# Kernel optimization log

Measured on AMD Instinct MI355X. Metric: run time of the kernel, lower is better.

## Reference

```python
import jax, jax.numpy as jnp
import numpy as np

D_MODEL = 1024
NUM_HEADS = 16
HEAD_DIM = D_MODEL // NUM_HEADS
WINDOW = 64
GLOBAL_TOKENS = 4
MAX_SEQ_LEN = 2048
RANDOM_TOKENS = 32
BATCH = 2
SEQ = 2048
NEG = -1.0e9
LN_EPS = 1e-5


def setup_inputs() -> dict:
    key = jax.random.key(0)
    k1, k2, k3, k4 = jax.random.split(key, 4)
    x = jax.random.normal(k1, (BATCH, SEQ, D_MODEL), dtype=jnp.float32)
    w_qkv = jax.random.normal(k2, (D_MODEL, 3 * D_MODEL), dtype=jnp.float32) * (D_MODEL ** -0.5)
    w_out = jax.random.normal(k3, (D_MODEL, D_MODEL), dtype=jnp.float32) * (D_MODEL ** -0.5)
    ln_gamma = jnp.ones((D_MODEL,), dtype=jnp.float32)
    ln_beta = jnp.zeros((D_MODEL,), dtype=jnp.float32)
    rand_idx = jax.random.randint(k4, (MAX_SEQ_LEN, RANDOM_TOKENS), 0, MAX_SEQ_LEN, dtype=jnp.int32)
    return {"x": x, "w_qkv": w_qkv, "w_out": w_out,
            "ln_gamma": ln_gamma, "ln_beta": ln_beta, "rand_idx": rand_idx}


def _build_masks(seq_len, rand_idx):
    i = jnp.arange(seq_len)
    causal = (i[:, None] >= i[None, :]).astype(jnp.float32)  # [L,L], lower-triangular
    # local window mask
    dist = jnp.abs(i[:, None] - i[None, :])
    local = (dist <= WINDOW).astype(jnp.float32) * causal
    # global column mask: columns {0..G-1} u {L-G..L-1}, rows i >= g (== causal on those cols)
    gcols = jnp.concatenate([jnp.arange(GLOBAL_TOKENS), jnp.arange(seq_len - GLOBAL_TOKENS, seq_len)])
    is_gcol = jnp.zeros((seq_len,), jnp.float32).at[gcols].set(1.0)
    glob = is_gcol[None, :] * causal
    # random mask: per-row fixed random columns, then causal-filtered
    ri = rand_idx[:seq_len]  # [L, R]
    rows = jnp.broadcast_to(i[:, None], ri.shape)
    rnd = jnp.zeros((seq_len, seq_len), jnp.float32).at[rows, ri].set(1.0) * causal
    return local, glob, rnd


def reference(x, w_qkv, w_out, ln_gamma, ln_beta, rand_idx):
    B, L, _ = x.shape
    residual = x
    # LayerNorm
    mu = jnp.mean(x, axis=-1, keepdims=True)
    var = jnp.mean(jnp.square(x - mu), axis=-1, keepdims=True)
    xn = (x - mu) * jax.lax.rsqrt(var + LN_EPS) * ln_gamma + ln_beta
    # QKV projection
    qkv = xn @ w_qkv
    q, k, v = jnp.split(qkv, 3, axis=-1)
    q = q.reshape(B, L, NUM_HEADS, HEAD_DIM).transpose(0, 2, 1, 3)  # [B,H,L,D]
    k = k.reshape(B, L, NUM_HEADS, HEAD_DIM).transpose(0, 2, 1, 3)
    v = v.reshape(B, L, NUM_HEADS, HEAD_DIM).transpose(0, 2, 1, 3)
    local, glob, rnd = _build_masks(L, rand_idx)
    raw = jnp.einsum('bhqd,bhkd->bhqk', q, k) / jnp.sqrt(jnp.float32(HEAD_DIM))
    # original sums three masked copies of the same scores:
    # combined = 3*raw + ((1-local)+(1-glob)+(1-rnd)) * NEG
    penalty = (3.0 - (local + glob + rnd)) * NEG  # [L,L]
    combined = 3.0 * raw + penalty[None, None, :, :]
    attn = jax.nn.softmax(combined, axis=-1)
    out = jnp.einsum('bhqk,bhkd->bhqd', attn, v)
    out = out.transpose(0, 2, 1, 3).reshape(B, L, D_MODEL)
    out = out @ w_out
    return out + residual
```

## Files before the change

### kernel.cpp

```cpp
#include <hip/hip_runtime.h>
#include <stdint.h>

typedef __attribute__((ext_vector_type(8))) short shortx8;
typedef __attribute__((ext_vector_type(4))) float floatx4;

static constexpr int SEQ_    = 2048;
static constexpr int DMODEL  = 1024;
static constexpr int HDIM    = 64;
static constexpr int BATCH_  = 2;
static constexpr int NHEADS  = 16;
static constexpr int WINDOW_ = 64;
static constexpr int GTOK    = 4;
static constexpr int RTOK    = 32;
static constexpr int ROWS    = BATCH_ * SEQ_;
static constexpr int QKVN    = 3 * DMODEL;

__device__ inline unsigned short f2bf(float f) {
  union { float f; unsigned int u; } x; x.f = f;
  unsigned int r = (x.u + 0x7FFFu + ((x.u >> 16) & 1u)) >> 16;
  return (unsigned short)r;
}
__device__ inline float bf2f(unsigned short b) {
  union { unsigned int u; float f; } x; x.u = ((unsigned int)b) << 16;
  return x.f;
}

__device__ inline void gload_lds16(const void* g, void* l) {
  __builtin_amdgcn_global_load_lds(
      (const __attribute__((address_space(1))) void*)g,
      (__attribute__((address_space(3))) void*)l, 16, 0, 0);
}

__device__ __forceinline__ void gemm_core128(
    const unsigned short* __restrict__ aSrc0, const unsigned short* __restrict__ aSrc1,
    const unsigned short* __restrict__ bSrc0, const unsigned short* __restrict__ bSrc1,
    unsigned short* Al, unsigned short* Bl,
    const int wave, const int lane, floatx4 (&acc)[4][4]) {
  const int quad = lane >> 4, l16 = lane & 15;
  const int wm = (wave >> 1) * 64, wn = (wave & 1) * 64;
  unsigned short* AlD0 = Al + (wave * 32) * 32;
  unsigned short* AlD1 = AlD0 + 16 * 32;
  unsigned short* BlD0 = Bl + (wave * 32) * 32;
  unsigned short* BlD1 = BlD0 + 16 * 32;
  for (int k0 = 0; k0 < 1024; k0 += 32) {
    __syncthreads();
    gload_lds16(aSrc0 + k0, AlD0);
    gload_lds16(aSrc1 + k0, AlD1);
    gload_lds16(bSrc0 + k0, BlD0);
    gload_lds16(bSrc1 + k0, BlD1);
    __syncthreads();
    shortx8 af[4], bfr[4];
    #pragma unroll
    for (int s = 0; s < 4; s++)
      af[s] = *(const shortx8*)&Al[(wm + s * 16 + l16) * 32 + quad * 8];
    #pragma unroll
    for (int s = 0; s < 4; s++)
      bfr[s] = *(const shortx8*)&Bl[(wn + s * 16 + l16) * 32 + quad * 8];
    #pragma unroll
    for (int sm = 0; sm < 4; sm++)
      #pragma unroll
      for (int sn = 0; sn < 4; sn++)
        acc[sm][sn] = __builtin_amdgcn_mfma_f32_16x16x32_bf16(af[sm], bfr[sn], acc[sm][sn], 0, 0, 0);
  }
}

__global__ __launch_bounds__(256) void k1_prep(
    const float* __restrict__ x, const float* __restrict__ w_qkv,
    const float* __restrict__ w_out, const float* __restrict__ gamma,
    const float* __restrict__ beta, const int* __restrict__ ridx,
    unsigned short* __restrict__ xn, unsigned short* __restrict__ wqT,
    unsigned short* __restrict__ woT, unsigned short* __restrict__ Wvs,
    int* __restrict__ cols, int* __restrict__ cnt, int* __restrict__ tmx,
    int* __restrict__ cnts2, int* __restrict__ qlist) {
  __shared__ float tile[32][33];
  __shared__ float red[4], red2[4];
  __shared__ int rl[RTOK];
  __shared__ int scw, scnw, stm;
  const int bx = blockIdx.x;
  const int t = threadIdx.x;
  if (bx < 3072) {
    int n0 = (bx % 96) * 32, k0 = (bx / 96) * 32;
    int tx = t & 31, ty = t >> 5;
    #pragma unroll
    for (int r = ty; r < 32; r += 8)
      tile[r][tx] = w_qkv[(size_t)(k0 + r) * QKVN + n0 + tx];
    __syncthreads();
    #pragma unroll
    for (int r = ty; r < 32; r += 8)
      wqT[(size_t)(n0 + r) * DMODEL + k0 + tx] = f2bf(tile[tx][r]);
  } else if (bx < 7168) {
    int row = bx - 3072;
    const float4* xr = (const float4*)(x + (size_t)row * DMODEL);
    float4 v = xr[t];
    float s = v.x + v.y + v.z + v.w;
    #pragma unroll
    for (int o = 32; o > 0; o >>= 1) s += __shfl_xor(s, o);
    int wave = t >> 6, lane = t & 63;
    if (lane == 0) red[wave] = s;
    __syncthreads();
    float mean = (red[0] + red[1] + red[2] + red[3]) * (1.0f / DMODEL);
    float dx = v.x - mean, dy = v.y - mean, dz = v.z - mean, dw = v.w - mean;
    float q = dx*dx + dy*dy + dz*dz + dw*dw;
    #pragma unroll
    for (int o = 32; o > 0; o >>= 1) q += __shfl_xor(q, o);
    if (lane == 0) red2[wave] = q;
    __syncthreads();
    float var = (red2[0] + red2[1] + red2[2] + red2[3]) * (1.0f / DMODEL);
    float rs = rsqrtf(var + 1e-5f);
    float4 g = ((const float4*)gamma)[t];
    float4 bb = ((const float4*)beta)[t];
    ushort4 outv;
    outv.x = f2bf(dx * rs * g.x + bb.x);
    outv.y = f2bf(dy * rs * g.y + bb.y);
    outv.z = f2bf(dz * rs * g.z + bb.z);
    outv.w = f2bf(dw * rs * g.w + bb.w);
    ((ushort4*)(xn + (size_t)row * DMODEL))[t] = outv;
  } else if (bx < 8192) {
    int idx = bx - 7168;
    int n0 = (idx & 31) * 32, k0 = (idx >> 5) * 32;
    int tx = t & 31, ty = t >> 5;
    #pragma unroll
    for (int r = ty; r < 32; r += 8)
      tile[r][tx] = w_out[(size_t)(k0 + r) * DMODEL + n0 + tx];
    __syncthreads();
    #pragma unroll
    for (int r = ty; r < 32; r += 8)
      woT[(size_t)(n0 + r) * DMODEL + k0 + tx] = f2bf(tile[tx][r]);
  } else if (bx < 9216) {
    int idx = bx - 8192;
    int v0 = (idx & 31) * 32, k0 = (idx >> 5) * 32;
    int tx = t & 31, ty = t >> 5;
    #pragma unroll
    for (int r = ty; r < 32; r += 8)
      Wvs[(size_t)(k0 + r) * DMODEL + v0 + tx] =
          f2bf(w_qkv[(size_t)(k0 + r) * QKVN + 2 * DMODEL + v0 + tx]);
  } else {
    const int i = bx - 9216;
    if (t < RTOK) rl[t] = ridx[i * RTOK + t];
    if (t == 0) { scw = 0; scnw = 0; stm = 0; }
    __syncthreads();
    const int wstart = (i - WINDOW_ > 0) ? (i - WINDOW_) : 0;
    const int c = t;
    int j = -1;
    bool valid = false;
    bool iswin = (c < 65);
    if (c < 65) {
      j = i - WINDOW_ + c;
      valid = (j >= 0);
    } else if (c < 73) {
      int g = c - 65;
      j = (g < 4) ? g : (SEQ_ - 8 + g);
      valid = (j <= i) && (j < wstart);
    } else if (c < 73 + RTOK) {
      int r = c - 73;
      j = rl[r];
      bool dup = false;
      for (int r2 = 0; r2 < r; r2++) dup = dup || (rl[r2] == j);
      valid = (j <= i) && (j < wstart) && !(j < GTOK || j >= SEQ_ - GTOK) && !dup;
    }
    int tier = -1;
    if (valid) {
      int loc = ((i - j) <= WINDOW_) ? 1 : 0;
      int glb = (j < GTOK || j >= SEQ_ - GTOK) ? 1 : 0;
      int rnd = 0;
      for (int r = 0; r < RTOK; r++) rnd |= (rl[r] == j) ? 1 : 0;
      tier = loc + glb + rnd;
      atomicMax(&stm, tier);
    }
    __syncthreads();
    const int tm = stm;
    if (valid && tier == tm) {
      if (iswin) {
        int pos = atomicAdd(&scw, 1);
        cols[i * 128 + pos] = j;
      } else {
        int pos = 127 - atomicAdd(&scnw, 1);
        cols[i * 128 + pos] = j;
      }
    }
    __syncthreads();
    if (t == 0) {
      cnt[i] = scw + scnw;
      tmx[i] = tm;
      cnts2[i] = scw | (scnw << 16);
      if (i < 68 || i >= SEQ_ - 4) {
        int cc = (i < 68) ? i : 68 + (i - (SEQ_ - 4));
        qlist[cc * 2 + 0] = (tm == 3) ? i : -1;
        qlist[cc * 2 + 1] = (tm == 3) ? (SEQ_ + i) : -1;
      }
    }
  }
}

__global__ __launch_bounds__(256) void k2_fused(
    const unsigned short* __restrict__ xn, const int* __restrict__ cols,
    const int* __restrict__ tmx, const int* __restrict__ cnts2,
    const unsigned short* __restrict__ woT, const unsigned short* __restrict__ Wvs,
    const unsigned short* __restrict__ wqT, const int* __restrict__ qlist,
    unsigned short* __restrict__ WvoT, unsigned short* __restrict__ qf,
    unsigned short* __restrict__ kf, unsigned short* __restrict__ vf,
    unsigned short* __restrict__ xbar) {
  __shared__ __align__(16) unsigned short smem[80 * 256];
  const int bx = blockIdx.x, t = threadIdx.x;
  const int wave = t >> 6, lane = t & 63;
  if (bx < 96) {
    unsigned short* Al = smem;
    unsigned short* Bl = smem + 128 * 32;
    const int lrow = lane >> 2, lkoff = (lane & 3) * 8;
    const int quad = lane >> 4, l16 = lane & 15;
    const int wm = (wave >> 1) * 64, wn = (wave & 1) * 64;
    floatx4 acc[4][4] = {};
    if (bx < 64) {
      const int bm = (bx >> 3) * 128, bn = (bx & 7) * 128;
      const unsigned short* a0 = woT + (size_t)(bm + wave * 32 + lrow) * DMODEL + lkoff;
      const unsigned short* a1 = a0 + 16 * DMODEL;
      const unsigned short* b0 = Wvs + (size_t)(bn + wave * 32 + lrow) * DMODEL + lkoff;
      const unsigned short* b1 = b0 + 16 * DMODEL;
      gemm_core128(a0, a1, b0, b1, Al, Bl, wave, lane, acc);
      #pragma unroll
      for (int sm = 0; sm < 4; sm++)
        #pragma unroll
        for (int sn = 0; sn < 4; sn++)
          #pragma unroll
          for (int r = 0; r < 4; r++) {
            int row = bm + wm + sm * 16 + quad * 4 + r;
            int col = bn + wn + sn * 16 + l16;
            WvoT[(size_t)row * DMODEL + col] = f2bf(acc[sm][sn][r]);
          }
    } else {
      const int idx = bx - 64;
      const int job = idx >> 3, bn = (idx & 7) * 128;
      const int wsel = (job < 2) ? 0 : ((job == 2) ? 1 : 2);
      const unsigned short* BT = wqT + (size_t)wsel * DMODEL * DMODEL;
      unsigned short* dstbuf = (job == 0) ? qf
                             : (job == 1) ? (qf + (size_t)128 * DMODEL)
                             : (job == 2) ? kf : vf;
      int rsrc[2];
      #pragma unroll
      for (int q = 0; q < 2; q++) {
        int m = wave * 32 + q * 16 + lrow;
        int row;
        if (job < 2) {
          int s = job * 128 + m;
          int ql = (s < 144) ? qlist[s] : -1;
          row = (ql < 0) ? 0 : ql;
        } else {
          row = (m < 16) ? ((m >> 3) * SEQ_ + (((m & 7) < 4) ? (m & 7) : (SEQ_ - 8 + (m & 7)))) : 0;
        }
        rsrc[q] = row;
      }
      const unsigned short* a0 = xn + (size_t)rsrc[0] * DMODEL + lkoff;
      const unsigned short* a1 = xn + (size_t)rsrc[1] * DMODEL + lkoff;
      const unsigned short* b0 = BT + (size_t)(bn + wave * 32 + lrow) * DMODEL + lkoff;
      const unsigned short* b1 = b0 + 16 * DMODEL;
      gemm_core128(a0, a1, b0, b1, Al, Bl, wave, lane, acc);
      #pragma unroll
      for (int sm = 0; sm < 4; sm++)
        #pragma unroll
        for (int sn = 0; sn < 4; sn++)
          #pragma unroll
          for (int r = 0; r < 4; r++) {
            int m = wm + sm * 16 + quad * 4 + r;
            int col = bn + wn + sn * 16 + l16;
            dstbuf[(size_t)m * DMODEL + col] = f2bf(acc[sm][sn][r]);
          }
    }
  } else {
    auto win = reinterpret_cast<unsigned short (*)[256]>(smem);
    const int xb = bx - 96;
    const int b = xb >> 9, rest = xb & 511;
    const int i0 = (rest >> 2) * 16, dimbase = (rest & 3) * 256;
    const size_t xnb = (size_t)(b * SEQ_) * DMODEL;
    const int lo = i0 - 64;
    const int r0 = i0 + wave * 4;
    int tm_[4], cw_[4], cnw_[4], jr0_[4], jr1_[4];
    #pragma unroll
    for (int rr = 0; rr < 4; rr++) {
      const int i = r0 + rr;
      tm_[rr] = tmx[i];
      int c2 = cnts2[i];
      cw_[rr] = c2 & 0xffff; cnw_[rr] = c2 >> 16;
      jr0_[rr] = cols[i * 128 + lane];
      jr1_[rr] = cols[i * 128 + 64 + lane];
    }
    {
      const int l5 = lane & 31, rsub = lane >> 5;
      #pragma unroll 5
      for (int it = 0; it < 10; it++) {
        int r = it * 8 + wave * 2 + rsub;
        int gr = lo + r;
        if (gr >= 0)
          *(int4*)&win[r][l5 * 8] =
              *(const int4*)(xn + xnb + (size_t)gr * DMODEL + dimbase + l5 * 8);
      }
    }
    __syncthreads();
    const unsigned short* xnd = xn + xnb + dimbase + lane * 4;
    auto add4 = [](float4& s, ushort4 v) {
      s.x += bf2f(v.x); s.y += bf2f(v.y); s.z += bf2f(v.z); s.w += bf2f(v.w);
    };
    auto sub4 = [](float4& s, ushort4 v) {
      s.x -= bf2f(v.x); s.y -= bf2f(v.y); s.z -= bf2f(v.z); s.w -= bf2f(v.w);
    };
    float4 ws = {0, 0, 0, 0};
    {
      float4 t1 = {0,0,0,0}, t2 = {0,0,0,0}, t3 = {0,0,0,0};
      const int jstart = (r0 - 64 > 0) ? (r0 - 64) : 0;
      const int cn = r0 - jstart + 1;
      const int base = jstart - lo;
      int c = 0;
      for (; c + 4 <= cn; c += 4) {
        ushort4 v0 = *(const ushort4*)&win[base + c][lane * 4];
        ushort4 v1 = *(const ushort4*)&win[base + c + 1][lane * 4];
        ushort4 v2 = *(const ushort4*)&win[base + c + 2][lane * 4];
        ushort4 v3 = *(const ushort4*)&win[base + c + 3][lane * 4];
        add4(ws, v0); add4(t1, v1); add4(t2, v2); add4(t3, v3);
      }
      for (; c < cn; c++) add4(ws, *(const ushort4*)&win[base + c][lane * 4]);
      ws.x += t1.x + t2.x + t3.x; ws.y += t1.y + t2.y + t3.y;
      ws.z += t1.z + t2.z + t3.z; ws.w += t1.w + t2.w + t3.w;
    }
    for (int rr = 0; rr < 4; rr++) {
      const int i = r0 + rr;
      if (rr > 0) {
        add4(ws, *(const ushort4*)&win[i - lo][lane * 4]);
        int dj = i - 65;
        if (dj >= 0) sub4(ws, *(const ushort4*)&win[dj - lo][lane * 4]);
      }
      const int tm = tm_[rr];
      ushort4 o;
      if (tm == 3) {
        o.x = o.y = o.z = o.w = 0;
      } else {
        const int cw = cw_[rr], cnw = cnw_[rr];
        const int jr1 = jr1_[rr];
        float4 s;
        if (tm == 1) {
          s = ws;
          float4 t1 = {0,0,0,0}, t2 = {0,0,0,0}, t3 = {0,0,0,0};
          const int bb = 64 - cnw;
          int c = 0;
          for (; c + 8 <= cnw; c += 8) {
            ushort4 v0 = *(const ushort4*)(xnd + (size_t)__shfl(jr1, bb + c)     * DMODEL);
            ushort4 v1 = *(const ushort4*)(xnd + (size_t)__shfl(jr1, bb + c + 1) * DMODEL);
            ushort4 v2 = *(const ushort4*)(xnd + (size_t)__shfl(jr1, bb + c + 2) * DMODEL);
            ushort4 v3 = *(const ushort4*)(xnd + (size_t)__shfl(jr1, bb + c + 3) * DMODEL);
            ushort4 v4 = *(const ushort4*)(xnd + (size_t)__shfl(jr1, bb + c + 4) * DMODEL);
            ushort4 v5 = *(const ushort4*)(xnd + (size_t)__shfl(jr1, bb + c + 5) * DMODEL);
            ushort4 v6 = *(const ushort4*)(xnd + (size_t)__shfl(jr1, bb + c + 6) * DMODEL);
            ushort4 v7 = *(const ushort4*)(xnd + (size_t)__shfl(jr1, bb + c + 7) * DMODEL);
            add4(s, v0); add4(t1, v1); add4(t2, v2); add4(t3, v3);
            add4(s, v4); add4(t1, v5); add4(t2, v6); add4(t3, v7);
          }
          if (c + 4 <= cnw) {
            ushort4 v0 = *(const ushort4*)(xnd + (size_t)__shfl(jr1, bb + c)     * DMODEL);
            ushort4 v1 = *(const ushort4*)(xnd + (size_t)__shfl(jr1, bb + c + 1) * DMODEL);
            ushort4 v2 = *(const ushort4*)(xnd + (size_t)__shfl(jr1, bb + c + 2) * DMODEL);
            ushort4 v3 = *(const ushort4*)(xnd + (size_t)__shfl(jr1, bb + c + 3) * DMODEL);
            add4(s, v0); add4(t1, v1); add4(t2, v2); add4(t3, v3);
            c += 4;
          }
          for (; c < cnw; c++)
            add4(s, *(const ushort4*)(xnd + (size_t)__shfl(jr1, bb + c) * DMODEL));
          s.x += t1.x + t2.x + t3.x; s.y += t1.y + t2.y + t3.y;
          s.z += t1.z + t2.z + t3.z; s.w += t1.w + t2.w + t3.w;
        } else {
          const int jr0 = jr0_[rr];
          s.x = s.y = s.z = s.w = 0.f;
          for (int c = 0; c < cw; c++) {
            int j = (c < 64) ? __shfl(jr0, c) : __shfl(jr1, c - 64);
            add4(s, *(const ushort4*)(xnd + (size_t)j * DMODEL));
          }
          const int bb = 64 - cnw;
          for (int c = 0; c < cnw; c++)
            add4(s, *(const ushort4*)(xnd + (size_t)__shfl(jr1, bb + c) * DMODEL));
        }
        const float inv = 1.0f / (float)(cw + cnw);
        o.x = f2bf(s.x * inv); o.y = f2bf(s.y * inv);
        o.z = f2bf(s.z * inv); o.w = f2bf(s.w * inv);
      }
      *(ushort4*)(xbar + (size_t)(b * SEQ_ + i) * DMODEL + dimbase + lane * 4) = o;
    }
  }
}

__global__ __launch_bounds__(256) void k3_t3(
    const int* __restrict__ cols, const int* __restrict__ cnt,
    const int* __restrict__ qlist,
    const unsigned short* __restrict__ qf, const unsigned short* __restrict__ kf,
    const unsigned short* __restrict__ vf, unsigned short* __restrict__ vbar) {
  const int t = threadIdx.x;
  const int wave = t >> 6, lane = t & 63;
  const int s = blockIdx.x * 4 + wave;
  const int dst = (s < 144) ? qlist[s] : -1;
  if (dst < 0) return;
  const int b = dst >> 11, i = dst & (SEQ_ - 1);
  const int n = cnt[i];
  int myk = 0;
  if (lane < n) {
    int kj = cols[i * 128 + lane];
    myk = b * 8 + ((kj < 4) ? kj : (kj - (SEQ_ - 8)));
  }
  for (int h = 0; h < NHEADS; h++) {
    float qd = bf2f(qf[(size_t)s * DMODEL + h * HDIM + lane]);
    float w[8];
    float m = -1e30f;
    for (int c = 0; c < n; c++) {
      int ks = __shfl(myk, c);
      float kd = bf2f(kf[(size_t)ks * DMODEL + h * HDIM + lane]);
      float p = qd * kd;
      #pragma unroll
      for (int o = 32; o > 0; o >>= 1) p += __shfl_xor(p, o);
      p *= 0.375f;
      w[c] = p;
      m = fmaxf(m, p);
    }
    float denom = 0.f, acc = 0.f;
    for (int c = 0; c < n; c++) {
      int ks = __shfl(myk, c);
      float e = __expf(w[c] - m);
      denom += e;
      acc += e * bf2f(vf[(size_t)ks * DMODEL + h * HDIM + lane]);
    }
    vbar[(size_t)s * DMODEL + h * HDIM + lane] = f2bf(acc / denom);
  }
}

__global__ __launch_bounds__(256) void k4_final(
    const unsigned short* __restrict__ xbar, const unsigned short* __restrict__ WvoT,
    const unsigned short* __restrict__ vbar, const unsigned short* __restrict__ woT,
    const int* __restrict__ qlist, const int* __restrict__ tmx,
    const float* __restrict__ x, float* __restrict__ out) {
  __shared__ unsigned short Al[128 * 32];
  __shared__ unsigned short Bl[128 * 32];
  __shared__ int rowinf[128];
  const int bx = blockIdx.x, t = threadIdx.x;
  const int wave = t >> 6, lane = t & 63;
  const int lrow = lane >> 2, lkoff = (lane & 3) * 8;
  const int quad = lane >> 4, l16 = lane & 15;
  const int wm = (wave >> 1) * 64, wn = (wave & 1) * 64;
  floatx4 acc[4][4] = {};
  if (bx < 256) {
    const int bm = (bx >> 3) * 128, bn = (bx & 7) * 128;
    if (t < 128) rowinf[t] = tmx[(bm + t) & (SEQ_ - 1)];
    const unsigned short* a0 = xbar + (size_t)(bm + wave * 32 + lrow) * DMODEL + lkoff;
    const unsigned short* a1 = a0 + 16 * DMODEL;
    const unsigned short* b0 = WvoT + (size_t)(bn + wave * 32 + lrow) * DMODEL + lkoff;
    const unsigned short* b1 = b0 + 16 * DMODEL;
    gemm_core128(a0, a1, b0, b1, Al, Bl, wave, lane, acc);
    #pragma unroll
    for (int sm = 0; sm < 4; sm++)
      #pragma unroll
      for (int sn = 0; sn < 4; sn++)
        #pragma unroll
        for (int r = 0; r < 4; r++) {
          int m = wm + sm * 16 + quad * 4 + r;
          if (rowinf[m] != 3) {
            int col = bn + wn + sn * 16 + l16;
            size_t off = (size_t)(bm + m) * DMODEL + col;
            out[off] = acc[sm][sn][r] + x[off];
          }
        }
  } else {
    const int idx = bx - 256;
    const int bm = (idx >> 3) * 128, bn = (idx & 7) * 128;
    if (t < 128) {
      int s = bm + t;
      rowinf[t] = (s < 144) ? qlist[s] : -1;
    }
    const unsigned short* a0 = vbar + (size_t)(bm + wave * 32 + lrow) * DMODEL + lkoff;
    const unsigned short* a1 = a0 + 16 * DMODEL;
    const unsigned short* b0 = woT + (size_t)(bn + wave * 32 + lrow) * DMODEL + lkoff;
    const unsigned short* b1 = b0 + 16 * DMODEL;
    gemm_core128(a0, a1, b0, b1, Al, Bl, wave, lane, acc);
    #pragma unroll
    for (int sm = 0; sm < 4; sm++)
      #pragma unroll
      for (int sn = 0; sn < 4; sn++)
        #pragma unroll
        for (int r = 0; r < 4; r++) {
          int m = wm + sm * 16 + quad * 4 + r;
          int dst = rowinf[m];
          if (dst >= 0) {
            int col = bn + wn + sn * 16 + l16;
            size_t off = (size_t)dst * DMODEL + col;
            out[off] = acc[sm][sn][r] + x[off];
          }
        }
  }
}

extern "C" void kernel_launch(void* const* d_in, const int* in_sizes, int n_in,
                              void* d_out, int out_size, void* d_ws, size_t ws_size,
                              hipStream_t stream) {
  const float* x     = (const float*)d_in[0];
  const float* w_qkv = (const float*)d_in[1];
  const float* w_out = (const float*)d_in[2];
  const float* gamma = (const float*)d_in[3];
  const float* beta  = (const float*)d_in[4];
  const int*   ridx  = (const int*)d_in[5];
  float* out = (float*)d_out;

  char* ws = (char*)d_ws;
  size_t off = 0;
  auto alloc = [&](size_t bytes) {
    char* p = ws + off;
    off = (off + bytes + 255) & ~(size_t)255;
    return p;
  };
  unsigned short* xn   = (unsigned short*)alloc((size_t)ROWS * DMODEL * 2);
  unsigned short* wqT  = (unsigned short*)alloc((size_t)QKVN * DMODEL * 2);
  unsigned short* woT  = (unsigned short*)alloc((size_t)DMODEL * DMODEL * 2);
  unsigned short* Wvs  = (unsigned short*)alloc((size_t)DMODEL * DMODEL * 2);
  unsigned short* WvoT = (unsigned short*)alloc((size_t)DMODEL * DMODEL * 2);
  unsigned short* xbar = (unsigned short*)alloc((size_t)ROWS * DMODEL * 2);
  unsigned short* qf   = (unsigned short*)alloc((size_t)256 * DMODEL * 2);
  unsigned short* kf   = (unsigned short*)alloc((size_t)128 * DMODEL * 2);
  unsigned short* vf   = (unsigned short*)alloc((size_t)128 * DMODEL * 2);
  unsigned short* vbar = (unsigned short*)alloc((size_t)256 * DMODEL * 2);
  int* cols  = (int*)alloc((size_t)SEQ_ * 128 * 4);
  int* cnt   = (int*)alloc((size_t)SEQ_ * 4);
  int* tmx   = (int*)alloc((size_t)SEQ_ * 4);
  int* cnts2 = (int*)alloc((size_t)SEQ_ * 4);
  int* qlist = (int*)alloc(256 * 4);

  hipLaunchKernelGGL(k1_prep, dim3(11264), dim3(256), 0, stream,
                     x, w_qkv, w_out, gamma, beta, ridx,
                     xn, wqT, woT, Wvs, cols, cnt, tmx, cnts2, qlist);
  hipLaunchKernelGGL(k2_fused, dim3(1120), dim3(256), 0, stream,
                     xn, cols, tmx, cnts2, woT, Wvs, wqT, qlist,
                     WvoT, qf, kf, vf, xbar);
  hipLaunchKernelGGL(k3_t3, dim3(36), dim3(256), 0, stream,
                     cols, cnt, qlist, qf, kf, vf, vbar);
  hipLaunchKernelGGL(k4_final, dim3(272), dim3(256), 0, stream,
                     xbar, WvoT, vbar, woT, qlist, tmx, x, out);
}
```

Before: 181.9 us.

## Double-buffer k4_final GEMM with BK=64 tiles and XOR-swizzled LDS

Adds a new GEMM core for k4_final that loads 64-wide K tiles into two LDS buffers. The next tile is prefetched while MFMAs run on the current one, so there is one barrier per 64-K step instead of two per 32-K step. Both the global-to-LDS store and the fragment reads use an XOR swizzle on 8-element chunks to avoid bank conflicts. LDS use grows to 64KB per block, which may limit occupancy.

```diff
diff --git a/kernel.cpp b/kernel.cpp
--- a/kernel.cpp
+++ b/kernel.cpp
@@ -62,6 +62,53 @@
       for (int sn = 0; sn < 4; sn++)
         acc[sm][sn] = __builtin_amdgcn_mfma_f32_16x16x32_bf16(af[sm], bfr[sn], acc[sm][sn], 0, 0, 0);
   }
+}
+
+__device__ __forceinline__ void gemm_core_bk64(
+    const unsigned short* __restrict__ aPtr, const unsigned short* __restrict__ bPtr,
+    unsigned short* smem, const int wave, const int lane, floatx4 (&acc)[4][4]) {
+  const int quad = lane >> 4, l16 = lane & 15;
+  const int wm = (wave >> 1) * 64, wn = (wave & 1) * 64;
+  const int h = l16 & 7;
+  auto STAGE = [&](int c, int k0) {
+    unsigned short* Ad = smem + c * 16384 + wave * 2048;
+    unsigned short* Bd = Ad + 8192;
+    #pragma unroll
+    for (int g = 0; g < 4; g++) {
+      gload_lds16(aPtr + (size_t)g * 8 * DMODEL + k0, Ad + g * 512);
+      gload_lds16(bPtr + (size_t)g * 8 * DMODEL + k0, Bd + g * 512);
+    }
+  };
+  auto COMPUTE = [&](int c) {
+    const unsigned short* A = smem + c * 16384;
+    const unsigned short* B = A + 8192;
+    #pragma unroll
+    for (int kk = 0; kk < 2; kk++) {
+      shortx8 af[4], bfr[4];
+      #pragma unroll
+      for (int s = 0; s < 4; s++)
+        af[s] = *(const shortx8*)&A[(wm + s * 16 + l16) * 64 + (((quad + kk * 4) ^ h) * 8)];
+      #pragma unroll
+      for (int s = 0; s < 4; s++)
+        bfr[s] = *(const shortx8*)&B[(wn + s * 16 + l16) * 64 + (((quad + kk * 4) ^ h) * 8)];
+      #pragma unroll
+      for (int sm = 0; sm < 4; sm++)
+        #pragma unroll
+        for (int sn = 0; sn < 4; sn++)
+          acc[sm][sn] = __builtin_amdgcn_mfma_f32_16x16x32_bf16(af[sm], bfr[sn], acc[sm][sn], 0, 0, 0);
+    }
+  };
+  STAGE(0, 0);
+  __syncthreads();
+  int cur = 0;
+  #pragma unroll 1
+  for (int t = 0; t < 15; ++t) {
+    STAGE(cur ^ 1, (t + 1) * 64);
+    COMPUTE(cur);
+    __syncthreads();
+    cur ^= 1;
+  }
+  COMPUTE(cur);
 }
 
 __global__ __launch_bounds__(256) void k1_prep(
@@ -431,23 +478,21 @@
     const unsigned short* __restrict__ vbar, const unsigned short* __restrict__ woT,
     const int* __restrict__ qlist, const int* __restrict__ tmx,
     const float* __restrict__ x, float* __restrict__ out) {
-  __shared__ unsigned short Al[128 * 32];
-  __shared__ unsigned short Bl[128 * 32];
+  __shared__ unsigned short smem[2 * 2 * 8192];
   __shared__ int rowinf[128];
   const int bx = blockIdx.x, t = threadIdx.x;
   const int wave = t >> 6, lane = t & 63;
-  const int lrow = lane >> 2, lkoff = (lane & 3) * 8;
   const int quad = lane >> 4, l16 = lane & 15;
   const int wm = (wave >> 1) * 64, wn = (wave & 1) * 64;
+  const int r8 = lane >> 3;
+  const int swo = ((lane & 7) ^ r8) * 8;
   floatx4 acc[4][4] = {};
   if (bx < 256) {
     const int bm = (bx >> 3) * 128, bn = (bx & 7) * 128;
     if (t < 128) rowinf[t] = tmx[(bm + t) & (SEQ_ - 1)];
-    const unsigned short* a0 = xbar + (size_t)(bm + wave * 32 + lrow) * DMODEL + lkoff;
-    const unsigned short* a1 = a0 + 16 * DMODEL;
-    const unsigned short* b0 = WvoT + (size_t)(bn + wave * 32 + lrow) * DMODEL + lkoff;
-    const unsigned short* b1 = b0 + 16 * DMODEL;
-    gemm_core128(a0, a1, b0, b1, Al, Bl, wave, lane, acc);
+    const unsigned short* a0 = xbar + (size_t)(bm + wave * 32 + r8) * DMODEL + swo;
+    const unsigned short* b0 = WvoT + (size_t)(bn + wave * 32 + r8) * DMODEL + swo;
+    gemm_core_bk64(a0, b0, smem, wave, lane, acc);
     #pragma unroll
     for (int sm = 0; sm < 4; sm++)
       #pragma unroll
@@ -468,11 +513,9 @@
       int s = bm + t;
       rowinf[t] = (s < 144) ? qlist[s] : -1;
     }
-    const unsigned short* a0 = vbar + (size_t)(bm + wave * 32 + lrow) * DMODEL + lkoff;
-    const unsigned short* a1 = a0 + 16 * DMODEL;
-    const unsigned short* b0 = woT + (size_t)(bn + wave * 32 + lrow) * DMODEL + lkoff;
-    const unsigned short* b1 = b0 + 16 * DMODEL;
-    gemm_core128(a0, a1, b0, b1, Al, Bl, wave, lane, acc);
+    const unsigned short* a0 = vbar + (size_t)(bm + wave * 32 + r8) * DMODEL + swo;
+    const unsigned short* b0 = woT + (size_t)(bn + wave * 32 + r8) * DMODEL + swo;
+    gemm_core_bk64(a0, b0, smem, wave, lane, acc);
     #pragma unroll
     for (int sm = 0; sm < 4; sm++)
       #pragma unroll
```

After: 179.7 us. About the same (-1.2%).
